# Performance work log

Hardware: AMD Instinct MI355X
Metric: run time of the kernel (lower is better)

Reference implementation:

```python
import jax, jax.numpy as jnp
import numpy as np

B, G, D, H, KD, E = 64, 512, 128, 8, 16, 128
NS = 20  # num_station


def _init_w(key, shape):
    stdv = 1.0 / np.sqrt(shape[-1]).astype(np.float32)
    return jax.random.uniform(key, shape, jnp.float32, -stdv, stdv)


def setup_inputs() -> dict:
    key = jax.random.key(0)
    ks = jax.random.split(key, 12)
    return {
        "q": jax.random.normal(ks[0], (B, G, D), jnp.float32),
        "h": jax.random.normal(ks[1], (B, G, D), jnp.float32),
        "W_query_depot": _init_w(ks[2], (H, D, KD)),
        "W_key_custom": _init_w(ks[3], (H, D, KD)),
        "W_val_custom": _init_w(ks[4], (H, D, KD)),
        "W_query_station": _init_w(ks[5], (H, D, KD)),
        "W_key_other": _init_w(ks[6], (H, D, KD)),
        "W_val_other": _init_w(ks[7], (H, D, KD)),
        "W_query_custom": _init_w(ks[8], (H, D, KD)),
        "W_key_all": _init_w(ks[9], (H, D, KD)),
        "W_val_all": _init_w(ks[10], (H, D, KD)),
        "W_out": _init_w(ks[11], (H, KD, E)),
        "num_station": NS,
    }


def _mha_block(q_seg, h_seg, Wq, Wk, Wv, norm):
    # q_seg: [B, Nq, D], h_seg: [B, Nk, D]; weights: [H, D, KD]
    Q = jnp.einsum('bqd,hdk->hbqk', q_seg, Wq)
    K = jnp.einsum('bnd,hdk->hbnk', h_seg, Wk)
    V = jnp.einsum('bnd,hdk->hbnk', h_seg, Wv)
    attn = jax.nn.softmax(norm * jnp.einsum('hbqk,hbnk->hbqn', Q, K), axis=-1)
    return jnp.einsum('hbqn,hbnk->hbqk', attn, V)  # [H, B, Nq, KD]


def reference(q, h, W_query_depot, W_key_custom, W_val_custom,
              W_query_station, W_key_other, W_val_other,
              W_query_custom, W_key_all, W_val_all, W_out, num_station):
    ns = num_station
    norm = 1.0 / np.sqrt(W_query_depot.shape[-1]).astype(np.float32)
    h_custom = h[:, 1 + ns:]                                        # customers
    h_other = jnp.concatenate([h[:, :1], h[:, 1 + ns:]], axis=1)    # depot + customers
    heads_depot = _mha_block(q[:, :1], h_custom,
                             W_query_depot, W_key_custom, W_val_custom, norm)
    heads_station = _mha_block(q[:, 1:1 + ns], h_other,
                               W_query_station, W_key_other, W_val_other, norm)
    heads_custom = _mha_block(q[:, 1 + ns:], h,
                              W_query_custom, W_key_all, W_val_all, norm)
    heads = jnp.concatenate([heads_depot, heads_station, heads_custom], axis=2)
    # final projection: mm([B*G, H*KD], [H*KD, E])
    return jnp.einsum('hbgk,hke->bge', heads, W_out)
```

## Files before the change

kernel.cpp:

```cpp
#include <hip/hip_runtime.h>
#include <hip/hip_bf16.h>

namespace {

typedef _Float16 v4h __attribute__((ext_vector_type(4)));
typedef __fp16   h2  __attribute__((ext_vector_type(2)));
typedef float    v4f __attribute__((ext_vector_type(4)));

constexpr int B = 64, G = 512, D = 128, H = 8, KD = 16, NS = 20;
constexpr float NORM = 0.25f;
constexpr float L2E  = 1.44269504088896f;
constexpr float MFIX = 16.0f;
constexpr int KP = 20;
constexpr int VP = 520;
constexpr int QCH = 256;

__device__ __forceinline__ v4f mfma16(v4h a, v4h b, v4f c) {
  return __builtin_amdgcn_mfma_f32_16x16x16f16(a, b, c, 0, 0, 0);
}
__device__ __forceinline__ v4h cvt4(float4 v) {
  h2 a = __builtin_amdgcn_cvt_pkrtz(v.x, v.y);
  h2 b = __builtin_amdgcn_cvt_pkrtz(v.z, v.w);
  return v4h{(_Float16)a[0], (_Float16)a[1], (_Float16)b[0], (_Float16)b[1]};
}
__device__ __forceinline__ void pexp(v4f s0, v4f s1, v4h& p0, v4h& p1) {
  h2 e01 = __builtin_amdgcn_cvt_pkrtz(__builtin_amdgcn_exp2f(s0[0]),
                                      __builtin_amdgcn_exp2f(s0[1]));
  h2 e23 = __builtin_amdgcn_cvt_pkrtz(__builtin_amdgcn_exp2f(s0[2]),
                                      __builtin_amdgcn_exp2f(s0[3]));
  h2 e45 = __builtin_amdgcn_cvt_pkrtz(__builtin_amdgcn_exp2f(s1[0]),
                                      __builtin_amdgcn_exp2f(s1[1]));
  h2 e67 = __builtin_amdgcn_cvt_pkrtz(__builtin_amdgcn_exp2f(s1[2]),
                                      __builtin_amdgcn_exp2f(s1[3]));
  p0 = {(_Float16)e01[0], (_Float16)e01[1], (_Float16)e23[0], (_Float16)e23[1]};
  p1 = {(_Float16)e45[0], (_Float16)e45[1], (_Float16)e67[0], (_Float16)e67[1]};
}

struct SM {
  char      ht[16384];
  _Float16  Kl[512 * KP];
  _Float16  Vt[16 * VP];
};

template<int SEG, bool PAIR>
__device__ __forceinline__ void attn_loop(const SM& sm, int g, int c,
                                          v4h qfA, v4h qfB,
                                          v4f& oA, v4f& laA, v4f& oB, v4f& laB)
{
  constexpr int Ln  = SEG == 0 ? G - 1 - NS : SEG == 1 ? G - NS : G;
  constexpr int NCH = (Ln + 31) / 32;
  const _Float16* Kb = sm.Kl + c * KP + 4 * g;
  const _Float16* Vb = sm.Vt + c * VP + 4 * g;
  const v4f mc = {-MFIX, -MFIX, -MFIX, -MFIX};
  const v4h ones = {(_Float16)1.f, (_Float16)1.f, (_Float16)1.f, (_Float16)1.f};

  v4h k0 = *(const v4h*)(Kb);
  v4h k1 = *(const v4h*)(Kb + 16 * KP);
  v4f s0A = mfma16(k0, qfA, mc), s1A = mfma16(k1, qfA, mc);
  v4f s0B, s1B;
  if constexpr (PAIR) { s0B = mfma16(k0, qfB, mc); s1B = mfma16(k1, qfB, mc); }

  #pragma unroll
  for (int ch = 0; ch < NCH; ++ch) {
    const int nb = ch * 32;
    const v4h v0 = *(const v4h*)(Vb + nb);
    const v4h v1 = *(const v4h*)(Vb + nb + 16);
    v4f n0A, n1A, n0B, n1B;
    if (ch + 1 < NCH) {
      k0 = *(const v4h*)(Kb + (nb + 32) * KP);
      k1 = *(const v4h*)(Kb + (nb + 48) * KP);
      n0A = mfma16(k0, qfA, mc); n1A = mfma16(k1, qfA, mc);
      if constexpr (PAIR) { n0B = mfma16(k0, qfB, mc); n1B = mfma16(k1, qfB, mc); }
    }
    if constexpr ((Ln & 31) != 0) {
      if (ch == NCH - 1) {
        #pragma unroll
        for (int r = 0; r < 4; ++r) {
          if (nb + 4 * g + r >= Ln)      { s0A[r] = -1e30f; if constexpr (PAIR) s0B[r] = -1e30f; }
          if (nb + 16 + 4 * g + r >= Ln) { s1A[r] = -1e30f; if constexpr (PAIR) s1B[r] = -1e30f; }
        }
      }
    }
    v4h p0, p1;
    pexp(s0A, s1A, p0, p1);
    oA  = mfma16(v0, p0, oA);
    oA  = mfma16(v1, p1, oA);
    laA = mfma16(ones, p0, laA);
    laA = mfma16(ones, p1, laA);
    if constexpr (PAIR) {
      pexp(s0B, s1B, p0, p1);
      oB  = mfma16(v0, p0, oB);
      oB  = mfma16(v1, p1, oB);
      laB = mfma16(ones, p0, laB);
      laB = mfma16(ones, p1, laB);
      s0B = n0B; s1B = n1B;
    }
    s0A = n0A; s1A = n1A;
  }
}

template<int SEG>
__device__ __forceinline__ void seg_body(
    int bid, const float* __restrict__ q, const float* __restrict__ hb,
    const float* __restrict__ Wq, const float* __restrict__ Wk,
    const float* __restrict__ Wv, float* __restrict__ heads, SM& sm)
{
  constexpr int Lq   = SEG == 0 ? 1 : SEG == 1 ? NS : G - 1 - NS;
  constexpr int QOFF = SEG == 0 ? 0 : SEG == 1 ? 1  : 1 + NS;
  constexpr int Ln   = SEG == 0 ? G - 1 - NS : SEG == 1 ? G - NS : G;
  constexpr int NQC  = (Lq + QCH - 1) / QCH;

  const int hh   = bid >> 6;
  const int b    = bid & 63;
  const int tid  = threadIdx.x;
  const int w    = tid >> 6;
  const int lane = tid & 63;
  const int g    = lane >> 4, c = lane & 15;

  float4 rg[4];

  {
    v4h wA[8];
    const float* Wt = (w < 4) ? Wk : Wv;
    #pragma unroll
    for (int dc = 0; dc < 8; ++dc)
      #pragma unroll
      for (int bb = 0; bb < 4; ++bb)
        wA[dc][bb] = (_Float16)Wt[((size_t)hh * D + dc * 16 + 4 * g + bb) * KD + c];

    const int sb = w & 3;
    #pragma unroll
    for (int i = 0; i < 4; ++i) {
      int idx = tid + i * 512, r = idx >> 5, jj = idx & 31;
      int nn = r < Ln ? r : Ln - 1;
      int hr;
      if (SEG == 0)      hr = nn + 1 + NS;
      else if (SEG == 1) hr = (nn == 0) ? 0 : nn + NS;
      else               hr = nn;
      rg[i] = ((const float4*)(hb + ((size_t)b * G + hr) * D))[jj];
    }
    for (int t = 0; t < 8; ++t) {
      __syncthreads();
      #pragma unroll
      for (int i = 0; i < 4; ++i) {
        int idx = tid + i * 512, r = idx >> 5, jj = idx & 31;
        *(v4h*)(sm.ht + r * 256 + ((8 * jj) ^ ((r & 7) << 4))) = cvt4(rg[i]);
      }
      if (t < 7) {
        #pragma unroll
        for (int i = 0; i < 4; ++i) {
          int idx = tid + i * 512, r = idx >> 5, jj = idx & 31;
          int n = (t + 1) * 64 + r;
          int nn = n < Ln ? n : Ln - 1;
          int hr;
          if (SEG == 0)      hr = nn + 1 + NS;
          else if (SEG == 1) hr = (nn == 0) ? 0 : nn + NS;
          else               hr = nn;
          rg[i] = ((const float4*)(hb + ((size_t)b * G + hr) * D))[jj];
        }
      }
      __syncthreads();
      const int base = t * 64;
      v4f acc = {0.f, 0.f, 0.f, 0.f};
      #pragma unroll
      for (int dc = 0; dc < 8; ++dc) {
        const v4h a = *(const v4h*)(sm.ht + (sb * 16 + c) * 256 +
                                    ((32 * dc + 8 * g) ^ ((c & 7) << 4)));
        acc = mfma16(a, wA[dc], acc);
      }
      if (w < 4) {
        #pragma unroll
        for (int r = 0; r < 4; ++r)
          sm.Kl[(base + sb * 16 + 4 * g + r) * KP + c] = (_Float16)acc[r];
      } else {
        v4h vv = {(_Float16)acc[0], (_Float16)acc[1], (_Float16)acc[2], (_Float16)acc[3]};
        *(v4h*)(sm.Vt + c * VP + base + sb * 16 + 4 * g) = vv;
      }
    }
  }

  for (int qc = 0; qc < NQC; ++qc) {
    const int qbase = qc * QCH;
    const int qcnt  = (Lq - qbase < QCH) ? (Lq - qbase) : QCH;
    const int nqt   = (qcnt + 15) >> 4;
    const int nri   = (qcnt + 63) >> 6;

    v4h wQ[8];
    #pragma unroll
    for (int dc = 0; dc < 8; ++dc)
      #pragma unroll
      for (int bb = 0; bb < 4; ++bb)
        wQ[dc][bb] = (_Float16)(Wq[((size_t)hh * D + dc * 16 + 4 * g + bb) * KD + c]
                                * (NORM * L2E));

    v4f accA = {0.f,0.f,0.f,0.f}, accB = {0.f,0.f,0.f,0.f};
    #pragma unroll
    for (int i = 0; i < 4; ++i) {
      int idx = tid + i * 512, r = idx >> 5, jj = idx & 31;
      int qs = qbase + r;
      int gq = QOFF + (qs < Lq ? qs : Lq - 1);
      rg[i] = ((const float4*)(q + ((size_t)b * G + gq) * D))[jj];
    }
    for (int ri = 0; ri < nri; ++ri) {
      __syncthreads();
      #pragma unroll
      for (int i = 0; i < 4; ++i) {
        int idx = tid + i * 512, r = idx >> 5, jj = idx & 31;
        *(v4h*)(sm.ht + r * 256 + ((8 * jj) ^ ((r & 7) << 4))) = cvt4(rg[i]);
      }
      if (ri + 1 < nri) {
        #pragma unroll
        for (int i = 0; i < 4; ++i) {
          int idx = tid + i * 512, r = idx >> 5, jj = idx & 31;
          int qs = qbase + (ri + 1) * 64 + r;
          int gq = QOFF + (qs < Lq ? qs : Lq - 1);
          rg[i] = ((const float4*)(q + ((size_t)b * G + gq) * D))[jj];
        }
      }
      __syncthreads();
      if ((w >> 2) == (ri & 1)) {
        v4f acc = {0.f, 0.f, 0.f, 0.f};
        const int sb = w & 3;
        #pragma unroll
        for (int dc = 0; dc < 8; ++dc) {
          const v4h a = *(const v4h*)(sm.ht + (sb * 16 + c) * 256 +
                                      ((32 * dc + 8 * g) ^ ((c & 7) << 4)));
          acc = mfma16(a, wQ[dc], acc);
        }
        if (ri < 2) accA = acc; else accB = acc;
      }
    }
    __syncthreads();

    const int t0 = w, tB = w + 8;
    const bool hasA = t0 < nqt, hasB = tB < nqt;
    if (hasA) {
      _Float16* sh = (_Float16*)(sm.ht + w * 2048);
      v4h qfA, qfB = {};
      #pragma unroll
      for (int r = 0; r < 4; ++r) sh[(4 * g + r) * 20 + c] = (_Float16)accA[r];
      if (hasB) {
        _Float16* sh2 = sh + 320;
        #pragma unroll
        for (int r = 0; r < 4; ++r) sh2[(4 * g + r) * 20 + c] = (_Float16)accB[r];
        qfA = *(const v4h*)(sh + c * 20 + 4 * g);
        qfB = *(const v4h*)(sh2 + c * 20 + 4 * g);
      } else {
        qfA = *(const v4h*)(sh + c * 20 + 4 * g);
      }
      v4f oA = {0.f,0.f,0.f,0.f}, laA = {0.f,0.f,0.f,0.f};
      v4f oB = {0.f,0.f,0.f,0.f}, laB = {0.f,0.f,0.f,0.f};
      if (hasB) attn_loop<SEG, true >(sm, g, c, qfA, qfB, oA, laA, oB, laB);
      else      attn_loop<SEG, false>(sm, g, c, qfA, qfA, oA, laA, oB, laB);
      {
        const float invA = 1.0f / laA[0];
        const int qloc = qbase + t0 * 16 + c;
        if (qloc < Lq) {
          float4 val = {oA[0]*invA, oA[1]*invA, oA[2]*invA, oA[3]*invA};
          *(float4*)(heads + ((size_t)b * G + QOFF + qloc) * 128 + hh * 16 + 4 * g) = val;
        }
      }
      if (hasB) {
        const float invB = 1.0f / laB[0];
        const int qloc = qbase + tB * 16 + c;
        if (qloc < Lq) {
          float4 val = {oB[0]*invB, oB[1]*invB, oB[2]*invB, oB[3]*invB};
          *(float4*)(heads + ((size_t)b * G + QOFF + qloc) * 128 + hh * 16 + 4 * g) = val;
        }
      }
    }
  }
}

__global__ __launch_bounds__(512, 4)
void fused_attn(const float* __restrict__ q, const float* __restrict__ hb,
                const float* __restrict__ Wqd, const float* __restrict__ Wkc,
                const float* __restrict__ Wvc, const float* __restrict__ Wqs,
                const float* __restrict__ Wko, const float* __restrict__ Wvo,
                const float* __restrict__ Wqc, const float* __restrict__ Wka,
                const float* __restrict__ Wva, float* __restrict__ heads)
{
  __shared__ SM sm;
  const int bid = blockIdx.x;
  if (bid < 512)       seg_body<2>(bid,        q, hb, Wqc, Wka, Wva, heads, sm);
  else if (bid < 1024) seg_body<1>(bid - 512,  q, hb, Wqs, Wko, Wvo, heads, sm);
  else                 seg_body<0>(bid - 1024, q, hb, Wqd, Wkc, Wvc, heads, sm);
}

__global__ __launch_bounds__(256)
void out_proj_kernel(float* __restrict__ data, const float* __restrict__ Wout)
{
  __shared__ _Float16 WlT[128 * 132];
  __shared__ _Float16 Ah [64 * 132];
  const int tid  = threadIdx.x;
  const int lane = tid & 63, w = tid >> 6;
  const int g = lane >> 4, c = lane & 15;
  const size_t rowbase = (size_t)blockIdx.x * 64;

  #pragma unroll
  for (int i = 0; i < 16; ++i) {
    int idx = tid + i * 256;
    int k = idx >> 5, c4 = (idx & 31) * 4;
    float4 v = ((const float4*)Wout)[idx];
    WlT[(c4 + 0) * 132 + k] = (_Float16)v.x;
    WlT[(c4 + 1) * 132 + k] = (_Float16)v.y;
    WlT[(c4 + 2) * 132 + k] = (_Float16)v.z;
    WlT[(c4 + 3) * 132 + k] = (_Float16)v.w;
  }
  #pragma unroll
  for (int i = 0; i < 8; ++i) {
    int idx = tid + i * 256;
    int r = idx >> 5, c4 = (idx & 31) * 4;
    float4 v = ((const float4*)(data + rowbase * 128))[idx];
    *(v4h*)(Ah + r * 132 + c4) = cvt4(v);
  }
  __syncthreads();

  v4h af[8];
  #pragma unroll
  for (int dc = 0; dc < 8; ++dc)
    af[dc] = *(const v4h*)(Ah + (w * 16 + c) * 132 + dc * 16 + 4 * g);
  #pragma unroll
  for (int ct = 0; ct < 8; ++ct) {
    v4f acc = {0.f, 0.f, 0.f, 0.f};
    #pragma unroll
    for (int dc = 0; dc < 8; ++dc) {
      const v4h bf = *(const v4h*)(WlT + (ct * 16 + c) * 132 + dc * 16 + 4 * g);
      acc = mfma16(af[dc], bf, acc);
    }
    #pragma unroll
    for (int r = 0; r < 4; ++r)
      data[(rowbase + w * 16 + 4 * g + r) * 128 + ct * 16 + c] = acc[r];
  }
}

}

extern "C" void kernel_launch(void* const* d_in, const int* in_sizes, int n_in,
                              void* d_out, int out_size, void* d_ws, size_t ws_size,
                              hipStream_t stream) {
  const float* q    = (const float*)d_in[0];
  const float* h    = (const float*)d_in[1];
  const float* Wqd  = (const float*)d_in[2];
  const float* Wkc  = (const float*)d_in[3];
  const float* Wvc  = (const float*)d_in[4];
  const float* Wqs  = (const float*)d_in[5];
  const float* Wko  = (const float*)d_in[6];
  const float* Wvo  = (const float*)d_in[7];
  const float* Wqc  = (const float*)d_in[8];
  const float* Wka  = (const float*)d_in[9];
  const float* Wva  = (const float*)d_in[10];
  const float* Wout = (const float*)d_in[11];
  float* out = (float*)d_out;

  fused_attn<<<3 * B * H, 512, 0, stream>>>(q, h, Wqd, Wkc, Wvc,
                                            Wqs, Wko, Wvo, Wqc, Wka, Wva, out);
  out_proj_kernel<<<G * B / 64, 256, 0, stream>>>(out, Wout);
}
```

Before: 66.45 us.

## Halve staging buffer, rotate projection tiles across waves, skip Q transpose via swapped MFMA

Halves the shared staging tile from 64 to 32 rows, which shrinks LDS use and the prefetch register array. The K/V projection now runs 16 smaller steps, with work rotated across waves. The Q projection swaps the MFMA operands so each result lands already transposed, which removes the LDS round-trip and a barrier used to reshape Q fragments. The aim is higher occupancy and fewer LDS ops, in exchange for twice as many barrier iterations and fewer waves busy per step.

```diff
diff --git a/kernel.cpp b/kernel.cpp
--- a/kernel.cpp
+++ b/kernel.cpp
@@ -21,6 +21,11 @@
 __device__ __forceinline__ v4h cvt4(float4 v) {
   h2 a = __builtin_amdgcn_cvt_pkrtz(v.x, v.y);
   h2 b = __builtin_amdgcn_cvt_pkrtz(v.z, v.w);
+  return v4h{(_Float16)a[0], (_Float16)a[1], (_Float16)b[0], (_Float16)b[1]};
+}
+__device__ __forceinline__ v4h cvtacc(v4f v) {
+  h2 a = __builtin_amdgcn_cvt_pkrtz(v[0], v[1]);
+  h2 b = __builtin_amdgcn_cvt_pkrtz(v[2], v[3]);
   return v4h{(_Float16)a[0], (_Float16)a[1], (_Float16)b[0], (_Float16)b[1]};
 }
 __device__ __forceinline__ void pexp(v4f s0, v4f s1, v4h& p0, v4h& p1) {
@@ -37,7 +42,7 @@
 }
 
 struct SM {
-  char      ht[16384];
+  char      ht[8192];
   _Float16  Kl[512 * KP];
   _Float16  Vt[16 * VP];
 };
@@ -117,7 +122,7 @@
   const int lane = tid & 63;
   const int g    = lane >> 4, c = lane & 15;
 
-  float4 rg[4];
+  float4 rg[2];
 
   {
     v4h wA[8];
@@ -128,9 +133,9 @@
       for (int bb = 0; bb < 4; ++bb)
         wA[dc][bb] = (_Float16)Wt[((size_t)hh * D + dc * 16 + 4 * g + bb) * KD + c];
 
-    const int sb = w & 3;
-    #pragma unroll
-    for (int i = 0; i < 4; ++i) {
+    const int wk = w & 3;
+    #pragma unroll
+    for (int i = 0; i < 2; ++i) {
       int idx = tid + i * 512, r = idx >> 5, jj = idx & 31;
       int nn = r < Ln ? r : Ln - 1;
       int hr;
@@ -139,18 +144,18 @@
       else               hr = nn;
       rg[i] = ((const float4*)(hb + ((size_t)b * G + hr) * D))[jj];
     }
-    for (int t = 0; t < 8; ++t) {
+    for (int t = 0; t < 16; ++t) {
       __syncthreads();
       #pragma unroll
-      for (int i = 0; i < 4; ++i) {
+      for (int i = 0; i < 2; ++i) {
         int idx = tid + i * 512, r = idx >> 5, jj = idx & 31;
         *(v4h*)(sm.ht + r * 256 + ((8 * jj) ^ ((r & 7) << 4))) = cvt4(rg[i]);
       }
-      if (t < 7) {
+      if (t < 15) {
         #pragma unroll
-        for (int i = 0; i < 4; ++i) {
+        for (int i = 0; i < 2; ++i) {
           int idx = tid + i * 512, r = idx >> 5, jj = idx & 31;
-          int n = (t + 1) * 64 + r;
+          int n = (t + 1) * 32 + r;
           int nn = n < Ln ? n : Ln - 1;
           int hr;
           if (SEG == 0)      hr = nn + 1 + NS;
@@ -160,21 +165,24 @@
         }
       }
       __syncthreads();
-      const int base = t * 64;
-      v4f acc = {0.f, 0.f, 0.f, 0.f};
-      #pragma unroll
-      for (int dc = 0; dc < 8; ++dc) {
-        const v4h a = *(const v4h*)(sm.ht + (sb * 16 + c) * 256 +
-                                    ((32 * dc + 8 * g) ^ ((c & 7) << 4)));
-        acc = mfma16(a, wA[dc], acc);
-      }
-      if (w < 4) {
+      const int sl = (wk - 2 * t) & 3;
+      if (sl < 2) {
+        const int tile = 2 * t + sl;
+        v4f acc = {0.f, 0.f, 0.f, 0.f};
         #pragma unroll
-        for (int r = 0; r < 4; ++r)
-          sm.Kl[(base + sb * 16 + 4 * g + r) * KP + c] = (_Float16)acc[r];
-      } else {
-        v4h vv = {(_Float16)acc[0], (_Float16)acc[1], (_Float16)acc[2], (_Float16)acc[3]};
-        *(v4h*)(sm.Vt + c * VP + base + sb * 16 + 4 * g) = vv;
+        for (int dc = 0; dc < 8; ++dc) {
+          const v4h a = *(const v4h*)(sm.ht + (sl * 16 + c) * 256 +
+                                      ((32 * dc + 8 * g) ^ ((c & 7) << 4)));
+          acc = mfma16(a, wA[dc], acc);
+        }
+        if (w < 4) {
+          #pragma unroll
+          for (int r = 0; r < 4; ++r)
+            sm.Kl[(tile * 16 + 4 * g + r) * KP + c] = (_Float16)acc[r];
+        } else {
+          v4h vv = {(_Float16)acc[0], (_Float16)acc[1], (_Float16)acc[2], (_Float16)acc[3]};
+          *(v4h*)(sm.Vt + c * VP + tile * 16 + 4 * g) = vv;
+        }
       }
     }
   }
@@ -183,7 +191,7 @@
     const int qbase = qc * QCH;
     const int qcnt  = (Lq - qbase < QCH) ? (Lq - qbase) : QCH;
     const int nqt   = (qcnt + 15) >> 4;
-    const int nri   = (qcnt + 63) >> 6;
+    const int nri   = (qcnt + 31) >> 5;
 
     v4h wQ[8];
     #pragma unroll
@@ -195,7 +203,7 @@
 
     v4f accA = {0.f,0.f,0.f,0.f}, accB = {0.f,0.f,0.f,0.f};
     #pragma unroll
-    for (int i = 0; i < 4; ++i) {
+    for (int i = 0; i < 2; ++i) {
       int idx = tid + i * 512, r = idx >> 5, jj = idx & 31;
       int qs = qbase + r;
       int gq = QOFF + (qs < Lq ? qs : Lq - 1);
@@ -204,50 +212,42 @@
     for (int ri = 0; ri < nri; ++ri) {
       __syncthreads();
       #pragma unroll
-      for (int i = 0; i < 4; ++i) {
+      for (int i = 0; i < 2; ++i) {
         int idx = tid + i * 512, r = idx >> 5, jj = idx & 31;
         *(v4h*)(sm.ht + r * 256 + ((8 * jj) ^ ((r & 7) << 4))) = cvt4(rg[i]);
       }
       if (ri + 1 < nri) {
         #pragma unroll
-        for (int i = 0; i < 4; ++i) {
+        for (int i = 0; i < 2; ++i) {
           int idx = tid + i * 512, r = idx >> 5, jj = idx & 31;
-          int qs = qbase + (ri + 1) * 64 + r;
+          int qs = qbase + (ri + 1) * 32 + r;
           int gq = QOFF + (qs < Lq ? qs : Lq - 1);
           rg[i] = ((const float4*)(q + ((size_t)b * G + gq) * D))[jj];
         }
       }
       __syncthreads();
-      if ((w >> 2) == (ri & 1)) {
-        v4f acc = {0.f, 0.f, 0.f, 0.f};
-        const int sb = w & 3;
-        #pragma unroll
-        for (int dc = 0; dc < 8; ++dc) {
-          const v4h a = *(const v4h*)(sm.ht + (sb * 16 + c) * 256 +
-                                      ((32 * dc + 8 * g) ^ ((c & 7) << 4)));
-          acc = mfma16(a, wQ[dc], acc);
-        }
-        if (ri < 2) accA = acc; else accB = acc;
-      }
-    }
-    __syncthreads();
+      const int sl = (w - 2 * ri) & 7;
+      if (sl < 2) {
+        const int t = 2 * ri + sl;
+        if (t < nqt) {
+          v4f acc = {0.f, 0.f, 0.f, 0.f};
+          #pragma unroll
+          for (int dc = 0; dc < 8; ++dc) {
+            const v4h a = *(const v4h*)(sm.ht + (sl * 16 + c) * 256 +
+                                        ((32 * dc + 8 * g) ^ ((c & 7) << 4)));
+            acc = mfma16(wQ[dc], a, acc);
+          }
+          if (t < 8) accA = acc; else accB = acc;
+        }
+      }
+    }
 
     const int t0 = w, tB = w + 8;
     const bool hasA = t0 < nqt, hasB = tB < nqt;
     if (hasA) {
-      _Float16* sh = (_Float16*)(sm.ht + w * 2048);
-      v4h qfA, qfB = {};
-      #pragma unroll
-      for (int r = 0; r < 4; ++r) sh[(4 * g + r) * 20 + c] = (_Float16)accA[r];
-      if (hasB) {
-        _Float16* sh2 = sh + 320;
-        #pragma unroll
-        for (int r = 0; r < 4; ++r) sh2[(4 * g + r) * 20 + c] = (_Float16)accB[r];
-        qfA = *(const v4h*)(sh + c * 20 + 4 * g);
-        qfB = *(const v4h*)(sh2 + c * 20 + 4 * g);
-      } else {
-        qfA = *(const v4h*)(sh + c * 20 + 4 * g);
-      }
+      v4h qfA = cvtacc(accA);
+      v4h qfB = {};
+      if (hasB) qfB = cvtacc(accB);
       v4f oA = {0.f,0.f,0.f,0.f}, laA = {0.f,0.f,0.f,0.f};
       v4f oB = {0.f,0.f,0.f,0.f}, laB = {0.f,0.f,0.f,0.f};
       if (hasB) attn_loop<SEG, true >(sm, g, c, qfA, qfB, oA, laA, oB, laB);
```

After: 68.46 us. 3.0% more time.
